# Kernel tuning notes

Hardware: AMD Instinct MI355X
Metric: run time of the kernel (lower is better)

Reference implementation:

```python
import jax, jax.numpy as jnp
import numpy as np

BN_EPS = 1e-5


def setup_inputs() -> dict:
    key = jax.random.key(0)
    k1, k2, k3, k4 = jax.random.split(key, 4)
    B, C, H, W = 16, 128, 128, 128
    x = jax.random.normal(k1, (B, C, H, W), dtype=jnp.float32)
    gamma = jax.random.normal(k2, (1,), dtype=jnp.float32)
    bn_weight = jax.random.uniform(k3, (C,), dtype=jnp.float32)
    bn_bias = jax.random.normal(k4, (C,), dtype=jnp.float32)
    return {"x": x, "gamma": gamma, "bn_weight": bn_weight, "bn_bias": bn_bias}


def reference(x, gamma, bn_weight, bn_bias):
    B, C, H, W = x.shape
    q = x.reshape(B, C, H * W)                      # proj_query: [B, C, HW]
    # energy[b, i, j] = <channel i, channel j>
    energy = jnp.einsum('bin,bjn->bij', q, q)       # [B, C, C]
    energy_new = jnp.max(energy, axis=-1, keepdims=True) - energy
    attention = jax.nn.softmax(energy_new, axis=-1)  # [B, C, C]
    out = jnp.einsum('bij,bjn->bin', attention, q)  # [B, C, HW]
    out = out.reshape(B, C, H, W)
    out = gamma * out
    # BatchNorm2d in training mode: batch statistics over (B, H, W) per channel
    mean = jnp.mean(out, axis=(0, 2, 3), keepdims=True)
    var = jnp.var(out, axis=(0, 2, 3), keepdims=True)  # biased variance
    out = (out - mean) * jax.lax.rsqrt(var + BN_EPS)
    out = out * bn_weight[None, :, None, None] + bn_bias[None, :, None, None]
    return out + x
```

## Files before the change

kernel.cpp:

```cpp
#include <hip/hip_runtime.h>

#define BB 16
#define CC 128
#define NN 16384
#define BN_EPS 1e-5f

typedef unsigned short u16;
typedef short short8 __attribute__((ext_vector_type(8)));
typedef float floatx4 __attribute__((ext_vector_type(4)));

__device__ inline float b2f(u16 u) {
    union { unsigned int i; float f; } c; c.i = ((unsigned int)u) << 16; return c.f;
}
__device__ inline u16 f2b(float f) {
    union { float f; unsigned int i; } c; c.f = f;
    unsigned int r = c.i + 0x7fffu + ((c.i >> 16) & 1u);
    return (u16)(r >> 16);
}

#define K1_LD 72
__global__ __launch_bounds__(256, 4) void k_gram(const float* __restrict__ x,
                                                 float* __restrict__ energy,
                                                 float* __restrict__ S)
{
    __shared__ u16 th[128 * K1_LD];
    __shared__ u16 tl[128 * K1_LD];
    const int rbid = blockIdx.x;
    const int xcd  = rbid & 7;
    const int li   = rbid >> 3;
    const int b    = xcd + 8 * (li >> 6);
    const int sub  = li & 63;
    const int rowhalf = sub & 1;
    const int k0   = (sub >> 1) * 512;
    const int t    = threadIdx.x;
    const int w = t >> 6, lane = t & 63, quad = lane >> 4, colL = lane & 15;

    floatx4 acc[8];
#pragma unroll
    for (int ct = 0; ct < 8; ++ct) acc[ct] = {0.f, 0.f, 0.f, 0.f};
    float rs[8];
#pragma unroll
    for (int it = 0; it < 8; ++it) rs[it] = 0.f;

    const float* xb = x + (size_t)b * CC * NN;
    const int rrow = t >> 4;
    const int c4   = t & 15;

    float4 v[8];
#pragma unroll
    for (int it = 0; it < 8; ++it)
        v[it] = *(const float4*)(xb + (size_t)(it * 16 + rrow) * NN + k0 + c4 * 4);

    const int arow = rowhalf * 64 + w * 16 + colL;
    for (int s = 0; s < 8; ++s) {
#pragma unroll
        for (int it = 0; it < 8; ++it) {
            const int row = it * 16 + rrow;
            float4 vv = v[it];
            if (s < 7)
                v[it] = *(const float4*)(xb + (size_t)row * NN + k0 + (s + 1) * 64 + c4 * 4);
            u16 h0 = f2b(vv.x), h1 = f2b(vv.y), h2 = f2b(vv.z), h3 = f2b(vv.w);
            uint2 hv, lv;
            hv.x = (unsigned)h0 | ((unsigned)h1 << 16);
            hv.y = (unsigned)h2 | ((unsigned)h3 << 16);
            lv.x = (unsigned)f2b(vv.x - b2f(h0)) | ((unsigned)f2b(vv.y - b2f(h1)) << 16);
            lv.y = (unsigned)f2b(vv.z - b2f(h2)) | ((unsigned)f2b(vv.w - b2f(h3)) << 16);
            *(uint2*)&th[row * K1_LD + c4 * 4] = hv;
            *(uint2*)&tl[row * K1_LD + c4 * 4] = lv;
            rs[it] += (vv.x + vv.y) + (vv.z + vv.w);
        }
        asm volatile("s_waitcnt lgkmcnt(0)" ::: "memory");
        __builtin_amdgcn_s_barrier();

#pragma unroll
        for (int ks2 = 0; ks2 < 2; ++ks2) {
            const int kk = ks2 * 32 + quad * 8;
            short8 ah = *(const short8*)&th[arow * K1_LD + kk];
            short8 al = *(const short8*)&tl[arow * K1_LD + kk];
#pragma unroll
            for (int ct = 0; ct < 8; ++ct) {
                short8 bh = *(const short8*)&th[(ct * 16 + colL) * K1_LD + kk];
                short8 bl = *(const short8*)&tl[(ct * 16 + colL) * K1_LD + kk];
                acc[ct] = __builtin_amdgcn_mfma_f32_16x16x32_bf16(ah, bh, acc[ct], 0, 0, 0);
                acc[ct] = __builtin_amdgcn_mfma_f32_16x16x32_bf16(al, bh, acc[ct], 0, 0, 0);
                acc[ct] = __builtin_amdgcn_mfma_f32_16x16x32_bf16(ah, bl, acc[ct], 0, 0, 0);
            }
        }
        asm volatile("s_waitcnt lgkmcnt(0)" ::: "memory");
        __builtin_amdgcn_s_barrier();
    }

    float* eb = energy + b * CC * CC;
    const int erow = rowhalf * 64 + w * 16 + quad * 4;
#pragma unroll
    for (int ct = 0; ct < 8; ++ct)
#pragma unroll
        for (int r = 0; r < 4; ++r)
            atomicAdd(&eb[(erow + r) * CC + ct * 16 + colL], acc[ct][r]);

    if (rowhalf == 0) {
#pragma unroll
        for (int it = 0; it < 8; ++it) {
            float ps = rs[it];
#pragma unroll
            for (int off = 8; off > 0; off >>= 1) ps += __shfl_down(ps, off, 16);
            if (colL == 0) atomicAdd(&S[b * CC + it * 16 + w * 4 + quad], ps);
        }
    }
}

__global__ __launch_bounds__(256) void k_soft(const float* __restrict__ energy,
                                              const float* __restrict__ S,
                                              u16* __restrict__ attb,
                                              float* __restrict__ meanacc,
                                              float* __restrict__ e2acc)
{
    const int b = blockIdx.x >> 7;
    const int i = blockIdx.x & 127;
    const int t = threadIdx.x;
    __shared__ float att[128];
    __shared__ float red[256];
    const float* E = energy + b * CC * CC;

    float e = (t < 128) ? E[i * CC + t] : 3.0e38f;
    red[t] = e; __syncthreads();
    for (int s2 = 128; s2 > 0; s2 >>= 1) { if (t < s2) red[t] = fminf(red[t], red[t + s2]); __syncthreads(); }
    float emin = red[0]; __syncthreads();

    float a = (t < 128) ? expf(emin - e) : 0.f;
    red[t] = a; __syncthreads();
    for (int s2 = 128; s2 > 0; s2 >>= 1) { if (t < s2) red[t] += red[t + s2]; __syncthreads(); }
    float Z = red[0]; __syncthreads();

    float attf = 0.f;
    if (t < 128) {
        u16 ab = f2b(a / Z);
        attf = b2f(ab);
        attb[((size_t)b * CC + i) * CC + t] = ab;
        att[t] = attf;
    }
    float mp = (t < 128) ? attf * S[b * CC + t] : 0.f;
    red[t] = mp; __syncthreads();
    for (int s2 = 128; s2 > 0; s2 >>= 1) { if (t < s2) red[t] += red[t + s2]; __syncthreads(); }
    if (t == 0) atomicAdd(&meanacc[i], red[0]);
    __syncthreads();

    const int j    = t & 127;
    const int half = t >> 7;
    const float* Ej = E + j * CC + half * 64;
    float inner = 0.f;
#pragma unroll 8
    for (int k = 0; k < 64; ++k) inner += att[half * 64 + k] * Ej[k];
    red[t] = inner; __syncthreads();
    float contrib = (t < 128) ? (red[t] + red[t + 128]) * att[t] : 0.f;
    __syncthreads();
    red[t] = contrib; __syncthreads();
    for (int s2 = 128; s2 > 0; s2 >>= 1) { if (t < s2) red[t] += red[t + s2]; __syncthreads(); }
    if (t == 0) atomicAdd(&e2acc[i], red[0]);
}

#define K3_LD 136
__global__ __launch_bounds__(256, 4) void k_out(const float* __restrict__ x,
                                                const u16* __restrict__ attb,
                                                const float* __restrict__ meanacc,
                                                const float* __restrict__ e2acc,
                                                const float* __restrict__ gamma,
                                                const float* __restrict__ bnw,
                                                const float* __restrict__ bnb,
                                                float* __restrict__ out)
{
    __shared__ u16 qT[128 * K3_LD];
    __shared__ float alpha[128];
    __shared__ float beta[128];
    const int b   = blockIdx.x >> 7;
    const int nn0 = (blockIdx.x & 127) * 128;
    const int t   = threadIdx.x;

    if (t < 128) {
        float g   = gamma[0];
        const float invBN = 1.f / (float)(BB * NN);
        float m   = g * meanacc[t] * invBN;
        float e2  = g * g * e2acc[t] * invBN;
        float var = e2 - m * m;
        float inv = rsqrtf(var + BN_EPS);
        float wv  = bnw[t];
        alpha[t] = g * wv * inv;
        beta[t]  = bnb[t] - m * wv * inv;
    }

    const float* xb = x + (size_t)b * CC * NN + nn0;
    const int n0 = (t & 31) * 4;
#pragma unroll
    for (int rep = 0; rep < 4; ++rep) {
        const int c0 = ((t >> 5) + rep * 8) * 4;
        float4 f0 = *(const float4*)(xb + (size_t)(c0 + 0) * NN + n0);
        float4 f1 = *(const float4*)(xb + (size_t)(c0 + 1) * NN + n0);
        float4 f2 = *(const float4*)(xb + (size_t)(c0 + 2) * NN + n0);
        float4 f3 = *(const float4*)(xb + (size_t)(c0 + 3) * NN + n0);
        const float fx[4] = {f0.x, f1.x, f2.x, f3.x};
        const float fy[4] = {f0.y, f1.y, f2.y, f3.y};
        const float fz[4] = {f0.z, f1.z, f2.z, f3.z};
        const float fw[4] = {f0.w, f1.w, f2.w, f3.w};
        const float* cols[4] = {fx, fy, fz, fw};
#pragma unroll
        for (int jn = 0; jn < 4; ++jn) {
            int n = n0 + jn;
            int g = ((c0 >> 3) + n) & 15;
            uint2 v;
            v.x = (unsigned)f2b(cols[jn][0]) | ((unsigned)f2b(cols[jn][1]) << 16);
            v.y = (unsigned)f2b(cols[jn][2]) | ((unsigned)f2b(cols[jn][3]) << 16);
            *(uint2*)&qT[n * K3_LD + g * 8 + (c0 & 7)] = v;
        }
    }
    __syncthreads();

    const int w = t >> 6, lane = t & 63, quad = lane >> 4, colL = lane & 15;
    const u16* ag = attb + (size_t)b * CC * CC;
    floatx4 acc[8][2];
#pragma unroll
    for (int rt = 0; rt < 8; ++rt) { acc[rt][0] = {0.f,0.f,0.f,0.f}; acc[rt][1] = {0.f,0.f,0.f,0.f}; }

#pragma unroll
    for (int ks = 0; ks < 4; ++ks) {
        const int kk = ks * 32 + quad * 8;
        const int n_a = w * 32 + colL;
        const int n_b = n_a + 16;
        short8 bf0 = *(const short8*)&qT[n_a * K3_LD + ((((kk) >> 3) + n_a) & 15) * 8];
        short8 bf1 = *(const short8*)&qT[n_b * K3_LD + ((((kk) >> 3) + n_b) & 15) * 8];
#pragma unroll
        for (int rt = 0; rt < 8; ++rt) {
            short8 af = *(const short8*)&ag[(rt * 16 + colL) * CC + kk];
            acc[rt][0] = __builtin_amdgcn_mfma_f32_16x16x32_bf16(af, bf0, acc[rt][0], 0, 0, 0);
            acc[rt][1] = __builtin_amdgcn_mfma_f32_16x16x32_bf16(af, bf1, acc[rt][1], 0, 0, 0);
        }
    }

    float* ob = out + (size_t)b * CC * NN + nn0;
#pragma unroll
    for (int rt = 0; rt < 8; ++rt)
#pragma unroll
        for (int ct = 0; ct < 2; ++ct)
#pragma unroll
            for (int r = 0; r < 4; ++r) {
                int chn = rt * 16 + quad * 4 + r;
                int nn  = w * 32 + ct * 16 + colL;
                float v = alpha[chn] * acc[rt][ct][r] + beta[chn]
                        + xb[(size_t)chn * NN + nn];
                ob[(size_t)chn * NN + nn] = v;
            }
}

extern "C" void kernel_launch(void* const* d_in, const int* in_sizes, int n_in,
                              void* d_out, int out_size, void* d_ws, size_t ws_size,
                              hipStream_t stream)
{
    const float* x     = (const float*)d_in[0];
    const float* gamma = (const float*)d_in[1];
    const float* bnw   = (const float*)d_in[2];
    const float* bnb   = (const float*)d_in[3];
    float* out = (float*)d_out;

    char* ws = (char*)d_ws;
    float* energy  = (float*)(ws);
    float* S       = (float*)(ws + 1048576);
    float* meanacc = (float*)(ws + 1056768);
    float* e2acc   = (float*)(ws + 1057280);
    u16*   attb    = (u16*)(ws + 1057792);

    hipMemsetAsync(ws, 0, 1057792, stream);
    hipLaunchKernelGGL(k_gram, dim3(1024), dim3(256), 0, stream, x, energy, S);
    hipLaunchKernelGGL(k_soft, dim3(2048), dim3(256), 0, stream, energy, S, attb, meanacc, e2acc);
    hipLaunchKernelGGL(k_out,  dim3(2048), dim3(256), 0, stream, x, attb, meanacc, e2acc, gamma, bnw, bnb, out);
}
```

Baseline: 341.0 us.

## Compute full 128x128 Gram tile per block with 512 threads

The Gram kernel previously split each K-chunk across two blocks by output row half, so each block converted and staged all 128 rows of x but used only half for its A operand. Each chunk is now handled by one 512-thread block with 8 waves tiling the full 128x128 output (2x4 MFMA tiles per wave). This halves redundant global loads and bf16 split conversions for the gram stage and reuses A fragments across more MFMAs. It also halves the grid and raises per-block register and LDS demands, which may reduce occupancy.

```diff
diff --git a/kernel.cpp b/kernel.cpp
--- a/kernel.cpp
+++ b/kernel.cpp
@@ -19,7 +19,7 @@
 }
 
 #define K1_LD 72
-__global__ __launch_bounds__(256, 4) void k_gram(const float* __restrict__ x,
+__global__ __launch_bounds__(512, 4) void k_gram(const float* __restrict__ x,
                                                  float* __restrict__ energy,
                                                  float* __restrict__ S)
 {
@@ -28,34 +28,36 @@
     const int rbid = blockIdx.x;
     const int xcd  = rbid & 7;
     const int li   = rbid >> 3;
-    const int b    = xcd + 8 * (li >> 6);
-    const int sub  = li & 63;
-    const int rowhalf = sub & 1;
-    const int k0   = (sub >> 1) * 512;
+    const int b    = xcd * 2 + (li >> 5);
+    const int k0   = (li & 31) * 512;
     const int t    = threadIdx.x;
     const int w = t >> 6, lane = t & 63, quad = lane >> 4, colL = lane & 15;
-
-    floatx4 acc[8];
-#pragma unroll
-    for (int ct = 0; ct < 8; ++ct) acc[ct] = {0.f, 0.f, 0.f, 0.f};
-    float rs[8];
-#pragma unroll
-    for (int it = 0; it < 8; ++it) rs[it] = 0.f;
+    const int w2 = w >> 1;
+    const int chf = w & 1;
+
+    floatx4 acc[2][4];
+#pragma unroll
+    for (int rt = 0; rt < 2; ++rt)
+#pragma unroll
+        for (int ct = 0; ct < 4; ++ct) acc[rt][ct] = {0.f, 0.f, 0.f, 0.f};
+    float rs[4];
+#pragma unroll
+    for (int it = 0; it < 4; ++it) rs[it] = 0.f;
 
     const float* xb = x + (size_t)b * CC * NN;
     const int rrow = t >> 4;
     const int c4   = t & 15;
 
-    float4 v[8];
-#pragma unroll
-    for (int it = 0; it < 8; ++it)
-        v[it] = *(const float4*)(xb + (size_t)(it * 16 + rrow) * NN + k0 + c4 * 4);
-
-    const int arow = rowhalf * 64 + w * 16 + colL;
+    float4 v[4];
+#pragma unroll
+    for (int it = 0; it < 4; ++it)
+        v[it] = *(const float4*)(xb + (size_t)(it * 32 + rrow) * NN + k0 + c4 * 4);
+
+    const int arow0 = w2 * 32 + colL;
     for (int s = 0; s < 8; ++s) {
 #pragma unroll
-        for (int it = 0; it < 8; ++it) {
-            const int row = it * 16 + rrow;
+        for (int it = 0; it < 4; ++it) {
+            const int row = it * 32 + rrow;
             float4 vv = v[it];
             if (s < 7)
                 v[it] = *(const float4*)(xb + (size_t)row * NN + k0 + (s + 1) * 64 + c4 * 4);
@@ -75,15 +77,21 @@
 #pragma unroll
         for (int ks2 = 0; ks2 < 2; ++ks2) {
             const int kk = ks2 * 32 + quad * 8;
-            short8 ah = *(const short8*)&th[arow * K1_LD + kk];
-            short8 al = *(const short8*)&tl[arow * K1_LD + kk];
-#pragma unroll
-            for (int ct = 0; ct < 8; ++ct) {
-                short8 bh = *(const short8*)&th[(ct * 16 + colL) * K1_LD + kk];
-                short8 bl = *(const short8*)&tl[(ct * 16 + colL) * K1_LD + kk];
-                acc[ct] = __builtin_amdgcn_mfma_f32_16x16x32_bf16(ah, bh, acc[ct], 0, 0, 0);
-                acc[ct] = __builtin_amdgcn_mfma_f32_16x16x32_bf16(al, bh, acc[ct], 0, 0, 0);
-                acc[ct] = __builtin_amdgcn_mfma_f32_16x16x32_bf16(ah, bl, acc[ct], 0, 0, 0);
+            short8 a0h = *(const short8*)&th[(arow0)      * K1_LD + kk];
+            short8 a0l = *(const short8*)&tl[(arow0)      * K1_LD + kk];
+            short8 a1h = *(const short8*)&th[(arow0 + 16) * K1_LD + kk];
+            short8 a1l = *(const short8*)&tl[(arow0 + 16) * K1_LD + kk];
+#pragma unroll
+            for (int ct = 0; ct < 4; ++ct) {
+                const int brow = chf * 64 + ct * 16 + colL;
+                short8 bh = *(const short8*)&th[brow * K1_LD + kk];
+                short8 bl = *(const short8*)&tl[brow * K1_LD + kk];
+                acc[0][ct] = __builtin_amdgcn_mfma_f32_16x16x32_bf16(a0h, bh, acc[0][ct], 0, 0, 0);
+                acc[1][ct] = __builtin_amdgcn_mfma_f32_16x16x32_bf16(a1h, bh, acc[1][ct], 0, 0, 0);
+                acc[0][ct] = __builtin_amdgcn_mfma_f32_16x16x32_bf16(a0l, bh, acc[0][ct], 0, 0, 0);
+                acc[1][ct] = __builtin_amdgcn_mfma_f32_16x16x32_bf16(a1l, bh, acc[1][ct], 0, 0, 0);
+                acc[0][ct] = __builtin_amdgcn_mfma_f32_16x16x32_bf16(a0h, bl, acc[0][ct], 0, 0, 0);
+                acc[1][ct] = __builtin_amdgcn_mfma_f32_16x16x32_bf16(a1h, bl, acc[1][ct], 0, 0, 0);
             }
         }
         asm volatile("s_waitcnt lgkmcnt(0)" ::: "memory");
@@ -91,21 +99,23 @@
     }
 
     float* eb = energy + b * CC * CC;
-    const int erow = rowhalf * 64 + w * 16 + quad * 4;
-#pragma unroll
-    for (int ct = 0; ct < 8; ++ct)
-#pragma unroll
-        for (int r = 0; r < 4; ++r)
-            atomicAdd(&eb[(erow + r) * CC + ct * 16 + colL], acc[ct][r]);
-
-    if (rowhalf == 0) {
-#pragma unroll
-        for (int it = 0; it < 8; ++it) {
-            float ps = rs[it];
-#pragma unroll
-            for (int off = 8; off > 0; off >>= 1) ps += __shfl_down(ps, off, 16);
-            if (colL == 0) atomicAdd(&S[b * CC + it * 16 + w * 4 + quad], ps);
-        }
+#pragma unroll
+    for (int rt = 0; rt < 2; ++rt)
+#pragma unroll
+        for (int ct = 0; ct < 4; ++ct)
+#pragma unroll
+            for (int r = 0; r < 4; ++r) {
+                int row = w2 * 32 + rt * 16 + quad * 4 + r;
+                int col = chf * 64 + ct * 16 + colL;
+                atomicAdd(&eb[row * CC + col], acc[rt][ct][r]);
+            }
+
+#pragma unroll
+    for (int it = 0; it < 4; ++it) {
+        float ps = rs[it];
+#pragma unroll
+        for (int off = 8; off > 0; off >>= 1) ps += __shfl_down(ps, off, 16);
+        if (c4 == 0) atomicAdd(&S[b * CC + it * 32 + rrow], ps);
     }
 }
 
@@ -268,7 +278,7 @@
     u16*   attb    = (u16*)(ws + 1057792);
 
     hipMemsetAsync(ws, 0, 1057792, stream);
-    hipLaunchKernelGGL(k_gram, dim3(1024), dim3(256), 0, stream, x, energy, S);
+    hipLaunchKernelGGL(k_gram, dim3(512), dim3(512), 0, stream, x, energy, S);
     hipLaunchKernelGGL(k_soft, dim3(2048), dim3(256), 0, stream, energy, S, attb, meanacc, e2acc);
     hipLaunchKernelGGL(k_out,  dim3(2048), dim3(256), 0, stream, x, attb, meanacc, e2acc, gamma, bnw, bnb, out);
 }
```

New measurement: 339.3 us. No clear change (-0.5%).
